# Performance work log

Hardware: AMD Instinct MI355X
Metric: run time of the kernel (lower is better)

## Reference

```python
import jax, jax.numpy as jnp
import numpy as np

DIM = 1024
N_HEADS = 16
HEAD_DIM = DIM // N_HEADS  # 64
FF_DIM = 4096
BATCH = 2
SEQ = 2048
EPS = 1e-8
ROPE_BASE = 10000.0


def _rope_cos_sin(seq_len, head_dim):
    # inv_freq: [head_dim//2]
    inv_freq = 1.0 / (ROPE_BASE ** (jnp.arange(0, head_dim, 2, dtype=jnp.float32) / head_dim))
    t = jnp.arange(seq_len, dtype=jnp.float32)
    freqs = jnp.einsum('i,j->ij', t, inv_freq)          # [S, D/2]
    emb = jnp.concatenate([freqs, freqs], axis=-1)       # [S, D]
    return jnp.cos(emb), jnp.sin(emb)


def _apply_rope(x, cos, sin):
    # x: [B, S, H, D]; cos/sin: [S, D] -> broadcast [1, S, 1, D]
    d2 = x.shape[-1] // 2
    x1, x2 = x[..., :d2], x[..., d2:]
    cos = cos[None, :, None, :]
    sin = sin[None, :, None, :]
    cos1, cos2 = cos[..., :d2], cos[..., d2:]
    sin1, sin2 = sin[..., :d2], sin[..., d2:]
    return jnp.concatenate([x1 * cos1 - x2 * sin1, x1 * sin2 + x2 * cos2], axis=-1)


def _rmsnorm(x, scale):
    # norm = ||x||_2 * d^{-1/2}; out = scale * x / (norm + eps)
    norm = jnp.sqrt(jnp.sum(x * x, axis=-1, keepdims=True)) * (x.shape[-1] ** -0.5)
    return scale * x / (norm + EPS)


def setup_inputs() -> dict:
    key = jax.random.key(0)
    ks = jax.random.split(key, 10)
    s = lambda fan_in: 1.0 / np.sqrt(fan_in)
    return {
        'x': jax.random.normal(ks[0], (BATCH, SEQ, DIM), dtype=jnp.float32),
        'w_qkv': jax.random.normal(ks[1], (DIM, 3 * DIM), dtype=jnp.float32) * s(DIM),
        'w_attn_out': jax.random.normal(ks[2], (DIM, DIM), dtype=jnp.float32) * s(DIM),
        'w_gate': jax.random.normal(ks[3], (DIM, FF_DIM), dtype=jnp.float32) * s(DIM),
        'b_gate': jax.random.normal(ks[4], (FF_DIM,), dtype=jnp.float32) * 0.01,
        'w_lin': jax.random.normal(ks[5], (DIM, FF_DIM), dtype=jnp.float32) * s(DIM),
        'b_lin': jax.random.normal(ks[6], (FF_DIM,), dtype=jnp.float32) * 0.01,
        'w_ff_out': jax.random.normal(ks[7], (FF_DIM, DIM), dtype=jnp.float32) * s(FF_DIM),
        'scale1': jnp.ones((DIM,), dtype=jnp.float32),
        'scale2': jnp.ones((DIM,), dtype=jnp.float32),
    }


def reference(x, w_qkv, w_attn_out, w_gate, b_gate, w_lin, b_lin, w_ff_out, scale1, scale2):
    B, S, _ = x.shape
    residual = x
    qkv = (x @ w_qkv).reshape(B, S, 3, N_HEADS, HEAD_DIM)
    q, k, v = qkv[:, :, 0], qkv[:, :, 1], qkv[:, :, 2]  # [B, S, H, D]
    cos, sin = _rope_cos_sin(S, HEAD_DIM)
    q = _apply_rope(q, cos, sin)
    k = _apply_rope(k, cos, sin)
    # attention scores [B, H, S, S]
    attn = jnp.einsum('bqhd,bkhd->bhqk', q, k) / np.sqrt(HEAD_DIM).astype(np.float32)
    attn = jax.nn.softmax(attn, axis=-1)
    out = jnp.einsum('bhqk,bkhd->bqhd', attn, v).reshape(B, S, DIM)
    out = out @ w_attn_out
    x = _rmsnorm(residual + out, scale1)
    residual = x
    ff = jax.nn.sigmoid(x @ w_gate + b_gate) * (x @ w_lin + b_lin)
    ff = ff @ w_ff_out
    x = _rmsnorm(residual + ff, scale2)
    return x
```

## Files before the change

kernel.cpp:

```cpp
#include <hip/hip_runtime.h>
#include <stdint.h>

#define DIMN 1024
#define NH 16
#define HD 64
#define FFN 4096
#define BBATCH 2
#define SSEQ 2048
#define MROWS (BBATCH*SSEQ)

typedef __bf16 bf16;
typedef __bf16 bf16x8 __attribute__((ext_vector_type(8)));
typedef __bf16 bf16x4 __attribute__((ext_vector_type(4)));
typedef float f32x4 __attribute__((ext_vector_type(4)));
typedef float f32x16 __attribute__((ext_vector_type(16)));
typedef uint32_t u32x4 __attribute__((ext_vector_type(4)));

#define AS1 __attribute__((address_space(1)))
#define AS3 __attribute__((address_space(3)))

__device__ __forceinline__ void gload16(const bf16* g, bf16* l) {
  __builtin_amdgcn_global_load_lds((AS1 const void*)g, (AS3 void*)l, 16, 0, 0);
}

__device__ __forceinline__ uint32_t pkbf(float a, float b) {
  union { bf16 h[2]; uint32_t u; } x;
  x.h[0] = (bf16)a; x.h[1] = (bf16)b;
  return x.u;
}

__global__ void rope_table_kernel(float* __restrict__ tab) {
  int i = blockIdx.x * blockDim.x + threadIdx.x;
  int s = i >> 5, d = i & 31;
  float invf = exp2f(-(float)d * 0.4152410118609203f);
  float fr = (float)s * invf;
  tab[s*64 + d]      = cosf(fr);
  tab[s*64 + 32 + d] = sinf(fr);
}

__global__ void cast_f32_bf16(const float* __restrict__ in, bf16* __restrict__ out, int n4) {
  int i = blockIdx.x * blockDim.x + threadIdx.x;
  if (i < n4) {
    f32x4 v = ((const f32x4*)in)[i];
    bf16x4 o = {(bf16)v.x, (bf16)v.y, (bf16)v.z, (bf16)v.w};
    ((bf16x4*)out)[i] = o;
  }
}

__global__ __launch_bounds__(256) void pack_wfrag(
    const float* __restrict__ W, bf16* __restrict__ WF, int K, int N) {
  int g = blockIdx.x * 4 + (threadIdx.x >> 6);
  int l = threadIdx.x & 63;
  int KT = K >> 5;
  int n  = g & 3;
  int kt = (g >> 2) % KT;
  int cb = (g >> 2) / KT;
  int c  = cb*64 + n*16 + (l & 15);
  int k0 = kt*32 + (l >> 4)*8;
  bf16x8 v;
  #pragma unroll
  for (int j = 0; j < 8; ++j) v[j] = (bf16)W[(size_t)(k0 + j)*N + c];
  *(bf16x8*)&WF[((size_t)g*64 + l)*8] = v;
}

template<int NP>
__global__ __launch_bounds__(256) void rmsnorm_sum_kernel(
    const float* __restrict__ parts, const float* __restrict__ resid,
    const float* __restrict__ sc,
    float* __restrict__ outf, bf16* __restrict__ outb) {
  int row = blockIdx.x;
  int tid = threadIdx.x;
  size_t off = (size_t)row * DIMN;
  f32x4 v = ((const f32x4*)(resid + off))[tid];
  #pragma unroll
  for (int p = 0; p < NP; ++p) {
    f32x4 a = ((const f32x4*)(parts + (size_t)p * MROWS * DIMN + off))[tid];
    v.x += a.x; v.y += a.y; v.z += a.z; v.w += a.w;
  }
  float ss = v.x*v.x + v.y*v.y + v.z*v.z + v.w*v.w;
  #pragma unroll
  for (int m = 1; m < 64; m <<= 1) ss += __shfl_xor(ss, m);
  __shared__ float red[4];
  if ((tid & 63) == 0) red[tid >> 6] = ss;
  __syncthreads();
  float tot = red[0] + red[1] + red[2] + red[3];
  float inv = 1.f / (sqrtf(tot) * 0.03125f + 1e-8f);
  f32x4 s4 = ((const f32x4*)sc)[tid];
  f32x4 o = {v.x*s4.x*inv, v.y*s4.y*inv, v.z*s4.z*inv, v.w*s4.w*inv};
  if (outf) ((f32x4*)(outf + off))[tid] = o;
  if (outb) {
    bf16x4 ob = {(bf16)o.x, (bf16)o.y, (bf16)o.z, (bf16)o.w};
    ((bf16x4*)(outb + off))[tid] = ob;
  }
}

template<int EPI>
__global__ void __launch_bounds__(256, 3) gemm_rw(
    const bf16* __restrict__ A, const bf16* __restrict__ WF,
    int M, int N, int K,
    void* __restrict__ o0, void* __restrict__ o1, void* __restrict__ o2,
    const void* __restrict__ a0) {
  __shared__ __align__(16) bf16 sh_a[2*4096];
  const int tid  = threadIdx.x;
  const int lane = tid & 63;
  const int wid  = tid >> 6;

  int gx  = gridDim.x;
  int bid = blockIdx.y * gx + blockIdx.x;
  int nwg = gx * gridDim.y;
  int cpx = nwg >> 3;
  int swz = (bid & 7) * cpx + (bid >> 3);
  int bxi = swz % gx, byi = swz / gx;

  const int m0 = byi * 128, n0 = bxi * 128;
  const int wm = (wid >> 1) * 64, wn = (wid & 1) * 64;

  const int kb = blockIdx.z;
  const int KC = K / (int)gridDim.z;
  const int KT = K >> 5;
  const int nt = KC >> 5;

  const int wcb = (n0 + wn) >> 6;
  const bf16* wf = WF + (size_t)wcb * KT * 2048;
  const bf16* a_base = A + (size_t)m0 * K + (size_t)kb * KC;

  auto stageA = [&](int kt, int buf) {
    #pragma unroll
    for (int i = 0; i < 2; ++i) {
      int idx = i*256 + tid;
      size_t go = (size_t)(idx >> 2)*K + (size_t)kt*32 + (idx & 3)*8;
      gload16(a_base + go, &sh_a[buf*4096 + idx*8]);
    }
  };
  auto ldW = [&](int kta, bf16x8* bb) {
    #pragma unroll
    for (int n = 0; n < 4; ++n)
      bb[n] = *(const bf16x8*)&wf[(size_t)kta*2048 + n*512 + lane*8];
  };

  f32x4 acc[4][4] = {};
  bf16x8 bcur[4], bnxt[4];

  ldW(kb*nt, bcur);
  stageA(0, 0);
  for (int t = 0; t < nt; ++t) {
    const int cb = t & 1;
    if (t + 1 < nt) {
      ldW(kb*nt + t + 1, bnxt);
      stageA(t+1, cb ^ 1);
      asm volatile("s_waitcnt vmcnt(6)" ::: "memory");
    } else {
      asm volatile("s_waitcnt vmcnt(0)" ::: "memory");
    }
    __builtin_amdgcn_sched_barrier(0);
    __builtin_amdgcn_s_barrier();
    __builtin_amdgcn_sched_barrier(0);

    const int lb = cb * 4096;
    bf16x8 af[4];
    #pragma unroll
    for (int m = 0; m < 4; ++m)
      af[m] = *(const bf16x8*)&sh_a[lb + (wm + m*16 + (lane & 15))*32 + (lane >> 4)*8];
    __builtin_amdgcn_s_setprio(1);
    #pragma unroll
    for (int m = 0; m < 4; ++m)
      #pragma unroll
      for (int n = 0; n < 4; ++n)
        acc[m][n] = __builtin_amdgcn_mfma_f32_16x16x32_bf16(af[m], bcur[n], acc[m][n], 0, 0, 0);
    __builtin_amdgcn_s_setprio(0);
    __builtin_amdgcn_sched_barrier(0);
    __builtin_amdgcn_s_barrier();
    if (t + 1 < nt) {
      #pragma unroll
      for (int n = 0; n < 4; ++n) bcur[n] = bnxt[n];
    }
  }

  const int rq = (lane >> 4) * 4;
  const int cl = lane & 15;

  if constexpr (EPI == 0) {
    bf16* q_p = (bf16*)o0; bf16* k_p = (bf16*)o1; bf16* v_p = (bf16*)o2;
    const float* rope = (const float*)a0;
    int sec = (n0 + wn) >> 10;
    int h   = ((n0 + wn) & 1023) >> 6;
    const float qsc = (sec == 0) ? 0.18033688011112042f : 1.0f;
    #pragma unroll
    for (int m = 0; m < 4; ++m) {
      #pragma unroll
      for (int reg = 0; reg < 4; ++reg) {
        int r  = m0 + wm + m*16 + rq + reg;
        int b_ = r >> 11, s_ = r & 2047;
        int tile = s_ >> 5;
        size_t tb = ((size_t)(b_*NH + h) * 64 + tile) * 2048;
        if (sec == 2) {
          int kvl = s_ & 31;
          int ks = kvl >> 4, hiv = (kvl >> 3) & 1, jv = kvl & 7;
          #pragma unroll
          for (int n = 0; n < 4; ++n) {
            int half = n >> 1;
            int qlv  = (n & 1) * 16 + cl;
            v_p[tb + (size_t)(ks*2 + half)*512 + (hiv*32 + qlv)*8 + jv] =
                (bf16)acc[m][n][reg];
          }
        } else {
          int qlt = s_ & 31;
          bf16* dst = (sec == 0 ? q_p : k_p);
          int lo = ((cl >> 3) * 32 + qlt) * 8 + (cl & 7);
          #pragma unroll
          for (int n = 0; n < 2; ++n) {
            int d1 = n*16 + cl;
            float c1 = rope[s_*64 + d1];
            float s1 = rope[s_*64 + 32 + d1];
            float x1 = acc[m][n][reg], x2 = acc[m][n+2][reg];
            dst[tb + (size_t)n*512 + lo]       = (bf16)((x1*c1 - x2*s1) * qsc);
            dst[tb + (size_t)(n+2)*512 + lo]   = (bf16)((x1*s1 + x2*c1) * qsc);
          }
        }
      }
    }
  } else if constexpr (EPI == 4) {
    float* op = (float*)o0 + (size_t)kb * M * N;
    #pragma unroll
    for (int m = 0; m < 4; ++m)
      #pragma unroll
      for (int n = 0; n < 4; ++n)
        #pragma unroll
        for (int reg = 0; reg < 4; ++reg) {
          int r = m0 + wm + m*16 + rq + reg;
          int c = n0 + wn + n*16 + cl;
          op[(size_t)r*N + c] = acc[m][n][reg];
        }
  }
}

__global__ void __launch_bounds__(256, 3) gemm_ffn1_rw(
    const bf16* __restrict__ A, const bf16* __restrict__ WgF,
    const bf16* __restrict__ WlF, int M, int N, int K,
    bf16* __restrict__ o0, const float* __restrict__ bgv,
    const float* __restrict__ blv) {
  __shared__ __align__(16) bf16 sh_a[2*4096];
  const int tid  = threadIdx.x;
  const int lane = tid & 63;
  const int wid  = tid >> 6;

  int gx  = gridDim.x;
  int bid = blockIdx.y * gx + blockIdx.x;
  int nwg = gx * gridDim.y;
  int cpx = nwg >> 3;
  int swz = (bid & 7) * cpx + (bid >> 3);
  int byi = swz & 31, bxi = swz >> 5;

  const int m0 = byi * 128, n0 = bxi * 64;
  const int wm = (wid >> 1) * 64, wn = (wid & 1) * 32;

  const int KT = K >> 5;
  const int fo = wn >> 4;
  const bf16* wg = WgF + (size_t)(n0 >> 6) * KT * 2048;
  const bf16* wl = WlF + (size_t)(n0 >> 6) * KT * 2048;
  const bf16* a_base = A + (size_t)m0 * K;

  auto stageA = [&](int kt, int buf) {
    #pragma unroll
    for (int i = 0; i < 2; ++i) {
      int idx = i*256 + tid;
      size_t go = (size_t)(idx >> 2)*K + (size_t)kt*32 + (idx & 3)*8;
      gload16(a_base + go, &sh_a[buf*4096 + idx*8]);
    }
  };
  auto ldW = [&](int kt, bf16x8* bb, bf16x8* cc) {
    #pragma unroll
    for (int n = 0; n < 2; ++n) {
      bb[n] = *(const bf16x8*)&wg[(size_t)kt*2048 + (fo+n)*512 + lane*8];
      cc[n] = *(const bf16x8*)&wl[(size_t)kt*2048 + (fo+n)*512 + lane*8];
    }
  };

  f32x4 acc[4][2] = {}, acc2[4][2] = {};
  bf16x8 wgA[2], wlA[2], wgB[2], wlB[2];

  auto compute = [&](int buf, bf16x8* bb, bf16x8* cc) {
    const int lb = buf * 4096;
    bf16x8 af[4];
    #pragma unroll
    for (int m = 0; m < 4; ++m)
      af[m] = *(const bf16x8*)&sh_a[lb + (wm + m*16 + (lane & 15))*32 + (lane >> 4)*8];
    __builtin_amdgcn_s_setprio(1);
    #pragma unroll
    for (int m = 0; m < 4; ++m)
      #pragma unroll
      for (int n = 0; n < 2; ++n) {
        acc [m][n] = __builtin_amdgcn_mfma_f32_16x16x32_bf16(af[m], bb[n], acc [m][n], 0, 0, 0);
        acc2[m][n] = __builtin_amdgcn_mfma_f32_16x16x32_bf16(af[m], cc[n], acc2[m][n], 0, 0, 0);
      }
    __builtin_amdgcn_s_setprio(0);
  };

  ldW(0, wgA, wlA);
  stageA(0, 0);
  for (int i = 0; i < KT/2; ++i) {
    const int t1 = 2*i + 1;
    ldW(t1, wgB, wlB);
    stageA(t1, 1);
    asm volatile("s_waitcnt vmcnt(6)" ::: "memory");
    __builtin_amdgcn_sched_barrier(0);
    __builtin_amdgcn_s_barrier();
    __builtin_amdgcn_sched_barrier(0);
    compute(0, wgA, wlA);
    __builtin_amdgcn_sched_barrier(0);
    __builtin_amdgcn_s_barrier();
    if (t1 + 1 < KT) {
      ldW(t1 + 1, wgA, wlA);
      stageA(t1 + 1, 0);
      asm volatile("s_waitcnt vmcnt(6)" ::: "memory");
    } else {
      asm volatile("s_waitcnt vmcnt(0)" ::: "memory");
    }
    __builtin_amdgcn_sched_barrier(0);
    __builtin_amdgcn_s_barrier();
    __builtin_amdgcn_sched_barrier(0);
    compute(1, wgB, wlB);
    __builtin_amdgcn_sched_barrier(0);
    __builtin_amdgcn_s_barrier();
  }

  const int rq = (lane >> 4) * 4;
  const int cl = lane & 15;
  #pragma unroll
  for (int m = 0; m < 4; ++m)
    #pragma unroll
    for (int n = 0; n < 2; ++n)
      #pragma unroll
      for (int reg = 0; reg < 4; ++reg) {
        int r = m0 + wm + m*16 + rq + reg;
        int c = n0 + wn + n*16 + cl;
        float gv = acc [m][n][reg] + bgv[c];
        float lv = acc2[m][n][reg] + blv[c];
        float sg = 1.f / (1.f + __expf(-gv));
        o0[(size_t)r*N + c] = (bf16)(sg * lv);
      }
}

__global__ void __launch_bounds__(256) attn_kernel(
    const bf16* __restrict__ qf_g, const bf16* __restrict__ kf_g,
    const bf16* __restrict__ vf_g, bf16* __restrict__ ao_g) {
  __shared__ __align__(16) bf16 lds_k[2*2048];
  __shared__ __align__(16) bf16 lds_v[2*2048];
  const int tid  = threadIdx.x;
  const int lane = tid & 63;
  const int qw   = tid >> 6;
  const int hi   = lane >> 5;
  const int ql   = lane & 31;
  const int bh   = blockIdx.y;
  const int b_   = bh >> 4, h = bh & 15;
  const int q0   = blockIdx.x * 128 + qw * 32;
  const int qt   = blockIdx.x * 4 + qw;

  const bf16* qtile = qf_g + ((size_t)bh*64 + qt) * 2048;
  const bf16* kbase = kf_g + (size_t)bh * 64 * 2048;
  const bf16* vbase = vf_g + (size_t)bh * 64 * 2048;

  bf16x8 qf[4];
  #pragma unroll
  for (int ds = 0; ds < 4; ++ds)
    qf[ds] = *(const bf16x8*)&qtile[ds*512 + lane*8];

  f32x16 o0 = {}, o1 = {};
  float lrun = 0.f;

  gload16(kbase + tid*8, &lds_k[tid*8]);
  gload16(vbase + tid*8, &lds_v[tid*8]);

  for (int t = 0; t < 64; ++t) {
    const int cur = (t & 1) * 2048;
    if (t < 63) {
      const int nxt = 2048 - cur;
      gload16(kbase + (size_t)(t+1)*2048 + tid*8, &lds_k[nxt + tid*8]);
      gload16(vbase + (size_t)(t+1)*2048 + tid*8, &lds_v[nxt + tid*8]);
      asm volatile("s_waitcnt vmcnt(2)" ::: "memory");
    } else {
      asm volatile("s_waitcnt vmcnt(0)" ::: "memory");
    }
    __builtin_amdgcn_sched_barrier(0);
    __builtin_amdgcn_s_barrier();
    __builtin_amdgcn_sched_barrier(0);

    f32x16 st = {};
    __builtin_amdgcn_s_setprio(1);
    #pragma unroll
    for (int ds = 0; ds < 4; ++ds) {
      bf16x8 kf = *(const bf16x8*)&lds_k[cur + ds*512 + lane*8];
      st = __builtin_amdgcn_mfma_f32_32x32x16_bf16(kf, qf[ds], st, 0, 0, 0);
    }
    __builtin_amdgcn_s_setprio(0);
    float p[16];
    float psum = 0.f;
    #pragma unroll
    for (int r = 0; r < 16; ++r) { p[r] = __builtin_amdgcn_exp2f(st[r]); psum += p[r]; }
    lrun += psum;

    uint32_t w0 = pkbf(p[0],p[1]),   w1 = pkbf(p[2],p[3]);
    uint32_t w2 = pkbf(p[4],p[5]),   w3 = pkbf(p[6],p[7]);
    uint32_t w4 = pkbf(p[8],p[9]),   w5 = pkbf(p[10],p[11]);
    uint32_t w6 = pkbf(p[12],p[13]), w7 = pkbf(p[14],p[15]);
    asm("v_permlane32_swap_b32 %0, %1" : "+v"(w0), "+v"(w2));
    asm("v_permlane32_swap_b32 %0, %1" : "+v"(w1), "+v"(w3));
    asm("v_permlane32_swap_b32 %0, %1" : "+v"(w4), "+v"(w6));
    asm("v_permlane32_swap_b32 %0, %1" : "+v"(w5), "+v"(w7));

    __builtin_amdgcn_s_setprio(1);
    {
      union { u32x4 u; bf16x8 b; } pu;
      u32x4 pwa = {w0, w1, w2, w3};
      pu.u = pwa;
      bf16x8 v0 = *(const bf16x8*)&lds_v[cur + 0*512 + lane*8];
      bf16x8 v1 = *(const bf16x8*)&lds_v[cur + 1*512 + lane*8];
      o0 = __builtin_amdgcn_mfma_f32_32x32x16_bf16(v0, pu.b, o0, 0, 0, 0);
      o1 = __builtin_amdgcn_mfma_f32_32x32x16_bf16(v1, pu.b, o1, 0, 0, 0);
      u32x4 pwb = {w4, w5, w6, w7};
      pu.u = pwb;
      bf16x8 v2 = *(const bf16x8*)&lds_v[cur + 2*512 + lane*8];
      bf16x8 v3 = *(const bf16x8*)&lds_v[cur + 3*512 + lane*8];
      o0 = __builtin_amdgcn_mfma_f32_32x32x16_bf16(v2, pu.b, o0, 0, 0, 0);
      o1 = __builtin_amdgcn_mfma_f32_32x32x16_bf16(v3, pu.b, o1, 0, 0, 0);
    }
    __builtin_amdgcn_s_setprio(0);

    __builtin_amdgcn_sched_barrier(0);
    __builtin_amdgcn_s_barrier();
    __builtin_amdgcn_sched_barrier(0);
  }

  lrun += __shfl_xor(lrun, 32);
  float inv = 1.f / lrun;
  bf16* aop = ao_g + ((size_t)(b_*SSEQ) + q0 + ql) * DIMN + h*HD;
  #pragma unroll
  for (int g = 0; g < 4; ++g) {
    int dbase = 8*g + 4*hi;
    bf16x4 w0 = {(bf16)(o0[4*g]*inv), (bf16)(o0[4*g+1]*inv),
                 (bf16)(o0[4*g+2]*inv), (bf16)(o0[4*g+3]*inv)};
    *(bf16x4*)&aop[dbase] = w0;
    bf16x4 w1 = {(bf16)(o1[4*g]*inv), (bf16)(o1[4*g+1]*inv),
                 (bf16)(o1[4*g+2]*inv), (bf16)(o1[4*g+3]*inv)};
    *(bf16x4*)&aop[32 + dbase] = w1;
  }
}

extern "C" void kernel_launch(void* const* d_in, const int* in_sizes, int n_in,
                              void* d_out, int out_size, void* d_ws, size_t ws_size,
                              hipStream_t stream) {
  const float* x      = (const float*)d_in[0];
  const float* w_qkv  = (const float*)d_in[1];
  const float* w_ao   = (const float*)d_in[2];
  const float* w_gate = (const float*)d_in[3];
  const float* b_gate = (const float*)d_in[4];
  const float* w_lin  = (const float*)d_in[5];
  const float* b_lin  = (const float*)d_in[6];
  const float* w_ffo  = (const float*)d_in[7];
  const float* scale1 = (const float*)d_in[8];
  const float* scale2 = (const float*)d_in[9];
  float* out = (float*)d_out;
  (void)ws_size; (void)in_sizes; (void)n_in; (void)out_size;

  uint8_t* ws = (uint8_t*)d_ws;
  bf16*  wt_ws   = (bf16*) (ws + 0);
  float* rope_ws = (float*)(ws + 8388608);
  bf16*  xb_ws   = (bf16*) (ws + 8912896);
  bf16*  ao_ws   = (bf16*) (ws + 8912896);
  bf16*  q_ws    = (bf16*) (ws + 17301504);
  bf16*  k_ws    = (bf16*) (ws + 25690112);
  bf16*  v_ws    = (bf16*) (ws + 34078720);
  float* p1_ws   = (float*)(ws + 17301504);
  bf16*  wt2_ws  = (bf16*) (ws + 50855936);
  bf16*  h1b_ws  = (bf16*) (ws + 84410368);
  bf16*  ffb_ws  = (bf16*) (ws + 8912896);
  float* p2_ws   = (float*)(ws + 42467328);
  float* h1f_ws  = (float*)(ws + 109576192);

  rope_table_kernel<<<256, 256, 0, stream>>>(rope_ws);
  cast_f32_bf16<<<4096, 256, 0, stream>>>(x, xb_ws, MROWS*DIMN/4);
  pack_wfrag<<<1536, 256, 0, stream>>>(w_qkv, wt_ws, DIMN, 3*DIMN);
  gemm_rw<0><<<dim3(24, 32), 256, 0, stream>>>(xb_ws, wt_ws, MROWS, 3*DIMN, DIMN,
                                               q_ws, k_ws, v_ws, rope_ws);
  attn_kernel<<<dim3(16, 32), 256, 0, stream>>>(q_ws, k_ws, v_ws, ao_ws);
  pack_wfrag<<<512, 256, 0, stream>>>(w_ao, wt_ws, DIMN, DIMN);
  gemm_rw<4><<<dim3(8, 32, 2), 256, 0, stream>>>(ao_ws, wt_ws, MROWS, DIMN, DIMN,
                                                 p1_ws, nullptr, nullptr, nullptr);
  rmsnorm_sum_kernel<2><<<MROWS, 256, 0, stream>>>(p1_ws, x, scale1, h1f_ws, h1b_ws);
  pack_wfrag<<<2048, 256, 0, stream>>>(w_gate, wt_ws, DIMN, FFN);
  pack_wfrag<<<2048, 256, 0, stream>>>(w_lin, wt2_ws, DIMN, FFN);
  gemm_ffn1_rw<<<dim3(64, 32), 256, 0, stream>>>(h1b_ws, wt_ws, wt2_ws, MROWS, FFN, DIMN,
                                                 ffb_ws, b_gate, b_lin);
  pack_wfrag<<<2048, 256, 0, stream>>>(w_ffo, wt_ws, FFN, DIMN);
  gemm_rw<4><<<dim3(8, 32, 4), 256, 0, stream>>>(ffb_ws, wt_ws, MROWS, DIMN, FFN,
                                                 p2_ws, nullptr, nullptr, nullptr);
  rmsnorm_sum_kernel<4><<<MROWS, 256, 0, stream>>>(p2_ws, h1f_ws, scale2, out, nullptr);
}
```

Before: 308.7 us.

## Split attention over two key halves and combine fp32 partials in new kernel

Adds a grid z dimension of 2 to the attention kernel, so each block processes only half of the key/value tiles. Each block writes unnormalized fp32 output partials and its row sums to workspace. A new combine kernel adds the two partials, divides by the summed row sums and writes bf16. The aim is to double the number of blocks for better CU occupancy and latency hiding. In exchange it adds an extra launch and a large fp32 partial write and read.

```diff
diff --git a/kernel.cpp b/kernel.cpp
--- a/kernel.cpp
+++ b/kernel.cpp
@@ -343,7 +343,8 @@
 
 __global__ void __launch_bounds__(256) attn_kernel(
     const bf16* __restrict__ qf_g, const bf16* __restrict__ kf_g,
-    const bf16* __restrict__ vf_g, bf16* __restrict__ ao_g) {
+    const bf16* __restrict__ vf_g, float* __restrict__ op_g,
+    float* __restrict__ lr_g) {
   __shared__ __align__(16) bf16 lds_k[2*2048];
   __shared__ __align__(16) bf16 lds_v[2*2048];
   const int tid  = threadIdx.x;
@@ -355,6 +356,8 @@
   const int b_   = bh >> 4, h = bh & 15;
   const int q0   = blockIdx.x * 128 + qw * 32;
   const int qt   = blockIdx.x * 4 + qw;
+  const int kb   = blockIdx.z;
+  const int t0   = kb * 32;
 
   const bf16* qtile = qf_g + ((size_t)bh*64 + qt) * 2048;
   const bf16* kbase = kf_g + (size_t)bh * 64 * 2048;
@@ -368,12 +371,12 @@
   f32x16 o0 = {}, o1 = {};
   float lrun = 0.f;
 
-  gload16(kbase + tid*8, &lds_k[tid*8]);
-  gload16(vbase + tid*8, &lds_v[tid*8]);
-
-  for (int t = 0; t < 64; ++t) {
+  gload16(kbase + (size_t)t0*2048 + tid*8, &lds_k[tid*8]);
+  gload16(vbase + (size_t)t0*2048 + tid*8, &lds_v[tid*8]);
+
+  for (int t = t0; t < t0 + 32; ++t) {
     const int cur = (t & 1) * 2048;
-    if (t < 63) {
+    if (t < t0 + 31) {
       const int nxt = 2048 - cur;
       gload16(kbase + (size_t)(t+1)*2048 + tid*8, &lds_k[nxt + tid*8]);
       gload16(vbase + (size_t)(t+1)*2048 + tid*8, &lds_v[nxt + tid*8]);
@@ -432,18 +435,35 @@
   }
 
   lrun += __shfl_xor(lrun, 32);
-  float inv = 1.f / lrun;
-  bf16* aop = ao_g + ((size_t)(b_*SSEQ) + q0 + ql) * DIMN + h*HD;
+  if (hi == 0)
+    lr_g[((size_t)(kb*32 + bh))*SSEQ + q0 + ql] = lrun;
+  float* opp = op_g + ((size_t)kb*MROWS + (size_t)(b_*SSEQ) + q0 + ql) * DIMN + h*HD;
   #pragma unroll
   for (int g = 0; g < 4; ++g) {
     int dbase = 8*g + 4*hi;
-    bf16x4 w0 = {(bf16)(o0[4*g]*inv), (bf16)(o0[4*g+1]*inv),
-                 (bf16)(o0[4*g+2]*inv), (bf16)(o0[4*g+3]*inv)};
-    *(bf16x4*)&aop[dbase] = w0;
-    bf16x4 w1 = {(bf16)(o1[4*g]*inv), (bf16)(o1[4*g+1]*inv),
-                 (bf16)(o1[4*g+2]*inv), (bf16)(o1[4*g+3]*inv)};
-    *(bf16x4*)&aop[32 + dbase] = w1;
-  }
+    f32x4 w0 = {o0[4*g], o0[4*g+1], o0[4*g+2], o0[4*g+3]};
+    *(f32x4*)&opp[dbase] = w0;
+    f32x4 w1 = {o1[4*g], o1[4*g+1], o1[4*g+2], o1[4*g+3]};
+    *(f32x4*)&opp[32 + dbase] = w1;
+  }
+}
+
+__global__ __launch_bounds__(256) void attn_combine(
+    const float* __restrict__ op, const float* __restrict__ lr,
+    bf16* __restrict__ ao) {
+  int r   = blockIdx.x;
+  int tid = threadIdx.x;
+  int b_  = r >> 11, s_ = r & 2047;
+  int c   = tid * 4;
+  int h   = c >> 6;
+  float l0 = lr[((size_t)(b_*NH + h))*SSEQ + s_];
+  float l1 = lr[(size_t)32*SSEQ + ((size_t)(b_*NH + h))*SSEQ + s_];
+  float inv = 1.f / (l0 + l1);
+  f32x4 a = *(const f32x4*)&op[(size_t)r*DIMN + c];
+  f32x4 b = *(const f32x4*)&op[(size_t)MROWS*DIMN + (size_t)r*DIMN + c];
+  bf16x4 o = {(bf16)((a.x+b.x)*inv), (bf16)((a.y+b.y)*inv),
+              (bf16)((a.z+b.z)*inv), (bf16)((a.w+b.w)*inv)};
+  *(bf16x4*)&ao[(size_t)r*DIMN + c] = o;
 }
 
 extern "C" void kernel_launch(void* const* d_in, const int* in_sizes, int n_in,
@@ -470,6 +490,8 @@
   bf16*  q_ws    = (bf16*) (ws + 17301504);
   bf16*  k_ws    = (bf16*) (ws + 25690112);
   bf16*  v_ws    = (bf16*) (ws + 34078720);
+  float* opar_ws = (float*)(ws + 42467328);
+  float* lr_ws   = (float*)(ws + 109576192);
   float* p1_ws   = (float*)(ws + 17301504);
   bf16*  wt2_ws  = (bf16*) (ws + 50855936);
   bf16*  h1b_ws  = (bf16*) (ws + 84410368);
@@ -482,7 +504,8 @@
   pack_wfrag<<<1536, 256, 0, stream>>>(w_qkv, wt_ws, DIMN, 3*DIMN);
   gemm_rw<0><<<dim3(24, 32), 256, 0, stream>>>(xb_ws, wt_ws, MROWS, 3*DIMN, DIMN,
                                                q_ws, k_ws, v_ws, rope_ws);
-  attn_kernel<<<dim3(16, 32), 256, 0, stream>>>(q_ws, k_ws, v_ws, ao_ws);
+  attn_kernel<<<dim3(16, 32, 2), 256, 0, stream>>>(q_ws, k_ws, v_ws, opar_ws, lr_ws);
+  attn_combine<<<MROWS, 256, 0, stream>>>(opar_ws, lr_ws, ao_ws);
   pack_wfrag<<<512, 256, 0, stream>>>(w_ao, wt_ws, DIMN, DIMN);
   gemm_rw<4><<<dim3(8, 32, 2), 256, 0, stream>>>(ao_ws, wt_ws, MROWS, DIMN, DIMN,
                                                  p1_ws, nullptr, nullptr, nullptr);
```

Result: no change. 312.2 us (+1.1%).

## Deepen A-tile LDS ring to 4 buffers, drop trailing barrier, swizzle LDS layout

Applied to the files above, without the earlier changes.

Both GEMM kernels now keep a 4-slot LDS ring for the A tile. Prefetch runs 2 to 3 K-steps ahead, and the second barrier per iteration is removed, since the slot being overwritten is no longer the one being read. The FFN1 kernel adds a 2-ahead weight register prefetch, unrolled by 4. An XOR swizzle on the 16-byte chunk column is applied to both the global source address and the LDS read address, to reduce bank conflicts. This quadruples shared memory per block and raises register use, which may lower occupancy under launch_bounds(256,3).

```diff
diff --git a/kernel.cpp b/kernel.cpp
--- a/kernel.cpp
+++ b/kernel.cpp
@@ -100,7 +100,7 @@
     int M, int N, int K,
     void* __restrict__ o0, void* __restrict__ o1, void* __restrict__ o2,
     const void* __restrict__ a0) {
-  __shared__ __align__(16) bf16 sh_a[2*4096];
+  __shared__ __align__(16) bf16 sh_a[4*4096];
   const int tid  = threadIdx.x;
   const int lane = tid & 63;
   const int wid  = tid >> 6;
@@ -128,7 +128,9 @@
     #pragma unroll
     for (int i = 0; i < 2; ++i) {
       int idx = i*256 + tid;
-      size_t go = (size_t)(idx >> 2)*K + (size_t)kt*32 + (idx & 3)*8;
+      int row = idx >> 2, slot = idx & 3;
+      int gch = slot ^ ((row >> 1) & 3);
+      size_t go = (size_t)row*K + (size_t)kt*32 + gch*8;
       gload16(a_base + go, &sh_a[buf*4096 + idx*8]);
     }
   };
@@ -138,16 +140,18 @@
       bb[n] = *(const bf16x8*)&wf[(size_t)kta*2048 + n*512 + lane*8];
   };
 
+  const int fr = lane & 15, fq = lane >> 4;
+  const int asl = (fq ^ ((fr >> 1) & 3)) * 8;
+
   f32x4 acc[4][4] = {};
   bf16x8 bcur[4], bnxt[4];
 
   ldW(kb*nt, bcur);
   stageA(0, 0);
+  stageA(1, 1);
   for (int t = 0; t < nt; ++t) {
-    const int cb = t & 1;
     if (t + 1 < nt) {
       ldW(kb*nt + t + 1, bnxt);
-      stageA(t+1, cb ^ 1);
       asm volatile("s_waitcnt vmcnt(6)" ::: "memory");
     } else {
       asm volatile("s_waitcnt vmcnt(0)" ::: "memory");
@@ -156,11 +160,11 @@
     __builtin_amdgcn_s_barrier();
     __builtin_amdgcn_sched_barrier(0);
 
-    const int lb = cb * 4096;
+    const int lb = (t & 3) * 4096;
     bf16x8 af[4];
     #pragma unroll
     for (int m = 0; m < 4; ++m)
-      af[m] = *(const bf16x8*)&sh_a[lb + (wm + m*16 + (lane & 15))*32 + (lane >> 4)*8];
+      af[m] = *(const bf16x8*)&sh_a[lb + (wm + m*16 + fr)*32 + asl];
     __builtin_amdgcn_s_setprio(1);
     #pragma unroll
     for (int m = 0; m < 4; ++m)
@@ -168,8 +172,7 @@
       for (int n = 0; n < 4; ++n)
         acc[m][n] = __builtin_amdgcn_mfma_f32_16x16x32_bf16(af[m], bcur[n], acc[m][n], 0, 0, 0);
     __builtin_amdgcn_s_setprio(0);
-    __builtin_amdgcn_sched_barrier(0);
-    __builtin_amdgcn_s_barrier();
+    if (t + 2 < nt) stageA(t + 2, (t + 2) & 3);
     if (t + 1 < nt) {
       #pragma unroll
       for (int n = 0; n < 4; ++n) bcur[n] = bnxt[n];
@@ -239,7 +242,7 @@
     const bf16* __restrict__ WlF, int M, int N, int K,
     bf16* __restrict__ o0, const float* __restrict__ bgv,
     const float* __restrict__ blv) {
-  __shared__ __align__(16) bf16 sh_a[2*4096];
+  __shared__ __align__(16) bf16 sh_a[4*4096];
   const int tid  = threadIdx.x;
   const int lane = tid & 63;
   const int wid  = tid >> 6;
@@ -264,7 +267,9 @@
     #pragma unroll
     for (int i = 0; i < 2; ++i) {
       int idx = i*256 + tid;
-      size_t go = (size_t)(idx >> 2)*K + (size_t)kt*32 + (idx & 3)*8;
+      int row = idx >> 2, slot = idx & 3;
+      int gch = slot ^ ((row >> 1) & 3);
+      size_t go = (size_t)row*K + (size_t)kt*32 + gch*8;
       gload16(a_base + go, &sh_a[buf*4096 + idx*8]);
     }
   };
@@ -276,15 +281,18 @@
     }
   };
 
+  const int fr = lane & 15, fq = lane >> 4;
+  const int asl = (fq ^ ((fr >> 1) & 3)) * 8;
+
   f32x4 acc[4][2] = {}, acc2[4][2] = {};
-  bf16x8 wgA[2], wlA[2], wgB[2], wlB[2];
+  bf16x8 wg0[2], wl0[2], wg1[2], wl1[2], wg2[2], wl2[2], wg3[2], wl3[2];
 
   auto compute = [&](int buf, bf16x8* bb, bf16x8* cc) {
     const int lb = buf * 4096;
     bf16x8 af[4];
     #pragma unroll
     for (int m = 0; m < 4; ++m)
-      af[m] = *(const bf16x8*)&sh_a[lb + (wm + m*16 + (lane & 15))*32 + (lane >> 4)*8];
+      af[m] = *(const bf16x8*)&sh_a[lb + (wm + m*16 + fr)*32 + asl];
     __builtin_amdgcn_s_setprio(1);
     #pragma unroll
     for (int m = 0; m < 4; ++m)
@@ -296,22 +304,11 @@
     __builtin_amdgcn_s_setprio(0);
   };
 
-  ldW(0, wgA, wlA);
-  stageA(0, 0);
-  for (int i = 0; i < KT/2; ++i) {
-    const int t1 = 2*i + 1;
-    ldW(t1, wgB, wlB);
-    stageA(t1, 1);
-    asm volatile("s_waitcnt vmcnt(6)" ::: "memory");
-    __builtin_amdgcn_sched_barrier(0);
-    __builtin_amdgcn_s_barrier();
-    __builtin_amdgcn_sched_barrier(0);
-    compute(0, wgA, wlA);
-    __builtin_amdgcn_sched_barrier(0);
-    __builtin_amdgcn_s_barrier();
-    if (t1 + 1 < KT) {
-      ldW(t1 + 1, wgA, wlA);
-      stageA(t1 + 1, 0);
+  auto tile = [&](int t, bf16x8* curG, bf16x8* curL, bf16x8* nxtG, bf16x8* nxtL) {
+    if (t + 2 < KT) {
+      ldW(t + 2, nxtG, nxtL);
+      asm volatile("s_waitcnt vmcnt(12)" ::: "memory");
+    } else if (t + 1 < KT) {
       asm volatile("s_waitcnt vmcnt(6)" ::: "memory");
     } else {
       asm volatile("s_waitcnt vmcnt(0)" ::: "memory");
@@ -319,9 +316,19 @@
     __builtin_amdgcn_sched_barrier(0);
     __builtin_amdgcn_s_barrier();
     __builtin_amdgcn_sched_barrier(0);
-    compute(1, wgB, wlB);
-    __builtin_amdgcn_sched_barrier(0);
-    __builtin_amdgcn_s_barrier();
+    compute(t & 3, curG, curL);
+    if (t + 3 < KT) stageA(t + 3, (t + 3) & 3);
+  };
+
+  ldW(0, wg0, wl0); stageA(0, 0);
+  ldW(1, wg1, wl1); stageA(1, 1);
+  stageA(2, 2);
+
+  for (int tb = 0; tb < KT; tb += 4) {
+    tile(tb + 0, wg0, wl0, wg2, wl2);
+    tile(tb + 1, wg1, wl1, wg3, wl3);
+    tile(tb + 2, wg2, wl2, wg0, wl0);
+    tile(tb + 3, wg3, wl3, wg1, wl1);
   }
 
   const int rq = (lane >> 4) * 4;
```

Result: slower. 425.5 us (+37.8%).
